# Optimization experiments

Hardware: AMD Instinct MI355X
Metric: run time of the kernel (lower is better)

Reference implementation:

```python
import jax, jax.numpy as jnp
import numpy as np

H = 12        # num_heads
BLOCK = 128   # sliding-window block_size (include_adjacent=True)
EPS = 1e-5


def layer_norm(x, s, b):
    m = x.mean(-1, keepdims=True)
    v = ((x - m) ** 2).mean(-1, keepdims=True)
    return (x - m) * jax.lax.rsqrt(v + EPS) * s + b


def setup_inputs() -> dict:
    key = jax.random.key(0)
    V, D, F, L, B, S, C = 32000, 768, 3072, 4, 8, 1024, 2
    ks = jax.random.split(key, 10)
    r = lambda k, shp: jax.random.normal(k, shp, dtype=jnp.float32) * 0.02
    return {
        "tokens": jax.random.randint(ks[0], (B, S), 0, V),
        "mask": jnp.ones((B, S), dtype=jnp.int32),
        "emb": r(ks[1], (V, D)),
        "in_w": r(ks[2], (L, 3 * D, D)),
        "in_b": jnp.zeros((L, 3 * D), jnp.float32),
        "out_w": r(ks[3], (L, D, D)),
        "out_b": jnp.zeros((L, D), jnp.float32),
        "ln1_s": jnp.ones((L, D), jnp.float32),
        "ln1_b": jnp.zeros((L, D), jnp.float32),
        "ln2_s": jnp.ones((L, D), jnp.float32),
        "ln2_b": jnp.zeros((L, D), jnp.float32),
        "ff_w1": r(ks[4], (L, F, D)),
        "ff_b1": jnp.zeros((L, F), jnp.float32),
        "ff_w2": r(ks[5], (L, D, F)),
        "ff_b2": jnp.zeros((L, D), jnp.float32),
        "pool_w": r(ks[6], (1, D)),
        "pool_b": jnp.zeros((1,), jnp.float32),
        "cls_ln_s": jnp.ones((D,), jnp.float32),
        "cls_ln_b": jnp.zeros((D,), jnp.float32),
        "cls_w1": r(ks[7], (D, D)),
        "cls_b1": jnp.zeros((D,), jnp.float32),
        "cls_w2": r(ks[8], (C, D)),
        "cls_b2": jnp.zeros((C,), jnp.float32),
    }


def reference(tokens, mask, emb, in_w, in_b, out_w, out_b, ln1_s, ln1_b, ln2_s, ln2_b,
              ff_w1, ff_b1, ff_w2, ff_b2, pool_w, pool_b, cls_ln_s, cls_ln_b,
              cls_w1, cls_b1, cls_w2, cls_b2):
    B, S = tokens.shape
    D = emb.shape[1]
    L = in_w.shape[0]
    hd = D // H
    neg = jnp.finfo(jnp.float32).min

    x = emb[tokens]  # [B,S,D]
    # sinusoidal positional encoding (eval mode: dropout = identity)
    pos = jnp.arange(S, dtype=jnp.float32)[:, None]
    div = jnp.exp(jnp.arange(0, D, 2, dtype=jnp.float32) * (-np.log(10000.0) / D))
    pe = (jnp.zeros((S, D), jnp.float32)
          .at[:, 0::2].set(jnp.sin(pos * div))
          .at[:, 1::2].set(jnp.cos(pos * div)))
    x = x + pe[None]

    idx = jnp.arange(S)
    band = jnp.abs(idx[None, :] - idx[:, None]) <= BLOCK        # [S,S] allowed band
    kpm = (mask != 0)                                            # [B,S] valid keys
    allowed = band[None] & kpm[:, None, :]                       # [B,S,S]

    all_w = []
    for l in range(L):
        h = layer_norm(x, ln1_s[l], ln1_b[l])
        qkv = h @ in_w[l].T + in_b[l]                            # [B,S,3D]
        q, k, v = jnp.split(qkv, 3, axis=-1)
        q = q.reshape(B, S, H, hd).transpose(0, 2, 1, 3) * (1.0 / np.sqrt(hd))
        k = k.reshape(B, S, H, hd).transpose(0, 2, 1, 3)
        v = v.reshape(B, S, H, hd).transpose(0, 2, 1, 3)
        scores = jnp.einsum('bhqd,bhkd->bhqk', q, k)             # [B,H,S,S]
        scores = jnp.where(allowed[:, None], scores, neg)
        w = jax.nn.softmax(scores, axis=-1)
        attn = jnp.einsum('bhqk,bhkd->bhqd', w, v)
        attn = attn.transpose(0, 2, 1, 3).reshape(B, S, D)
        attn = attn @ out_w[l].T + out_b[l]
        x = x + attn
        h2 = layer_norm(x, ln2_s[l], ln2_b[l])
        ff = jax.nn.gelu(h2 @ ff_w1[l].T + ff_b1[l], approximate=False)
        ff = ff @ ff_w2[l].T + ff_b2[l]
        x = x + ff
        all_w.append(w.mean(axis=1))                             # head-averaged [B,S,S]

    # attention pooling
    sc = (x @ pool_w.T + pool_b)[..., 0]                         # [B,S]
    sc = jnp.where(mask == 0, neg, sc)
    pw = jax.nn.softmax(sc, axis=-1)[..., None]
    pooled = jnp.sum(pw * x, axis=1)                             # [B,D]
    pooled = jnp.tanh(pooled)
    c = layer_norm(pooled, cls_ln_s, cls_ln_b)
    c = jnp.tanh(c @ cls_w1.T + cls_b1)
    out = c @ cls_w2.T + cls_b2                                  # [B,2]
    return out, jnp.stack(all_w)
```

## Files before the change

### kernel.cpp

```cpp
#include <hip/hip_runtime.h>
#include <math.h>

#define S_LEN 1024
#define D_MODEL 768
#define NHEAD 12
#define NEG_INF -3.4028234663852886e38f

#define QT 32
#define KB 288

typedef _Float16 f16x8 __attribute__((ext_vector_type(8)));
typedef __attribute__((ext_vector_type(4))) float f32x4;

typedef const __attribute__((address_space(1))) unsigned int ga_u32;
typedef __attribute__((address_space(3))) unsigned int ls_u32;
__device__ __forceinline__ void gload16(const void* g, void* l) {
  __builtin_amdgcn_global_load_lds((ga_u32*)g, (ls_u32*)l, 16, 0, 0);
}

__device__ __forceinline__ float gelu_exact(float v) {
  return 0.5f * v * (1.0f + erff(v * 0.7071067811865475f));
}
__device__ __forceinline__ unsigned short f2h(float f) {
  union { _Float16 h; unsigned short u; } x; x.h = (_Float16)f; return x.u;
}

__global__ __launch_bounds__(256) void embed_kernel(
    const int* __restrict__ tok, const float* __restrict__ emb,
    float* __restrict__ X, int total) {
  int i = blockIdx.x * 256 + threadIdx.x;
  if (i >= total) return;
  int d = i % D_MODEL;
  int bs = i / D_MODEL;
  int s = bs & (S_LEN - 1);
  int t = tok[bs];
  float div = expf((float)(d & ~1) * (-9.210340371976184f / 768.0f));
  float ang = (float)s * div;
  float pe = (d & 1) ? cosf(ang) : sinf(ang);
  X[i] = emb[(size_t)t * D_MODEL + d] + pe;
}

__global__ __launch_bounds__(256) void cvt_w_h(
    const float* __restrict__ W, unsigned short* __restrict__ H, int n4) {
  int i = blockIdx.x * 256 + threadIdx.x;
  if (i >= n4) return;
  float4 w = ((const float4*)W)[i];
  ushort4 h;
  h.x = f2h(w.x); h.y = f2h(w.y); h.z = f2h(w.z); h.w = f2h(w.w);
  ((ushort4*)H)[i] = h;
}

__global__ __launch_bounds__(256) void ln_kernel(
    const float* __restrict__ X, const float* __restrict__ gam,
    const float* __restrict__ bet, unsigned short* __restrict__ Y) {
  __shared__ float scratch[4];
  const int row = blockIdx.x;
  const int tid = threadIdx.x;
  const float* xr = X + (size_t)row * D_MODEL;
  float v0 = xr[tid], v1 = xr[tid + 256], v2 = xr[tid + 512];
  float s = v0 + v1 + v2;
#pragma unroll
  for (int o = 32; o; o >>= 1) s += __shfl_xor(s, o, 64);
  if ((tid & 63) == 0) scratch[tid >> 6] = s;
  __syncthreads();
  float mean = (scratch[0] + scratch[1] + scratch[2] + scratch[3]) * (1.0f / 768.0f);
  __syncthreads();
  float d0 = v0 - mean, d1 = v1 - mean, d2 = v2 - mean;
  float ss = d0 * d0 + d1 * d1 + d2 * d2;
#pragma unroll
  for (int o = 32; o; o >>= 1) ss += __shfl_xor(ss, o, 64);
  if ((tid & 63) == 0) scratch[tid >> 6] = ss;
  __syncthreads();
  float var = (scratch[0] + scratch[1] + scratch[2] + scratch[3]) * (1.0f / 768.0f);
  float rstd = rsqrtf(var + 1e-5f);
  unsigned short* yr = Y + (size_t)row * D_MODEL;
  yr[tid]       = f2h(d0 * rstd * gam[tid]       + bet[tid]);
  yr[tid + 256] = f2h(d1 * rstd * gam[tid + 256] + bet[tid + 256]);
  yr[tid + 512] = f2h(d2 * rstd * gam[tid + 512] + bet[tid + 512]);
}

template <int EPI>
__global__ __launch_bounds__(256) void gemm128(
    const unsigned short* __restrict__ A, const unsigned short* __restrict__ W,
    const float* __restrict__ bias, void* __restrict__ Cv,
    int N, int K, int NX) {
  __shared__ __align__(16) unsigned short SH[24576];
  const int tid = threadIdx.x;
  const int nwg = gridDim.x;
  const int wg = ((blockIdx.x & 7) * (nwg >> 3)) + (blockIdx.x >> 3);
  const int SX = NX >> 1;
  const int st = wg >> 4, w16 = wg & 15;
  const int ty = (st / SX) * 8 + (w16 >> 1);
  const int tx = (st % SX) * 2 + (w16 & 1);
  const int m0 = ty << 7, n0 = tx << 7;
  const int wave = tid >> 6, lane = tid & 63;
  const int wr = (wave >> 1) << 6, wc = (wave & 1) << 6;
  const int lq = lane >> 4, lr = lane & 15;
  const int rA0 = (wave << 5) + (lane >> 2);
  const int rA1 = rA0 + 16;
  const int sl = lane & 3;
  const size_t gA0 = (size_t)(m0 + rA0) * K + ((sl ^ ((rA0 >> 1) & 3)) << 3);
  const size_t gA1 = (size_t)(m0 + rA1) * K + ((sl ^ ((rA1 >> 1) & 3)) << 3);
  const size_t gB0 = (size_t)(n0 + rA0) * K + ((sl ^ ((rA0 >> 1) & 3)) << 3);
  const size_t gB1 = (size_t)(n0 + rA1) * K + ((sl ^ ((rA1 >> 1) & 3)) << 3);
  const int lws = wave << 10;

  const int nt = K >> 5;
  auto stage = [&](int buf, int t) {
    unsigned short* base = SH + (buf << 13);
    const int kk = t << 5;
    gload16(A + gA0 + kk, base + lws);
    gload16(A + gA1 + kk, base + lws + 512);
    gload16(W + gB0 + kk, base + 4096 + lws);
    gload16(W + gB1 + kk, base + 4096 + lws + 512);
  };
  stage(0, 0);
  stage(1, 1);

  f32x4 acc[4][4] = {};
  int cb = 0;
  for (int t = 0; t < nt; ++t) {
    if (t + 1 < nt) {
      asm volatile("s_waitcnt vmcnt(4)" ::: "memory");
    } else {
      asm volatile("s_waitcnt vmcnt(0)" ::: "memory");
    }
    __builtin_amdgcn_s_barrier();
    __builtin_amdgcn_sched_barrier(0);
    const unsigned short* As = SH + (cb << 13);
    const unsigned short* Bs = As + 4096;
    f16x8 af[4], bq[4];
#pragma unroll
    for (int i = 0; i < 4; ++i) {
      int r = wr + (i << 4) + lr;
      af[i] = *(const f16x8*)&As[r * 32 + ((lq ^ ((r >> 1) & 3)) << 3)];
    }
#pragma unroll
    for (int j = 0; j < 4; ++j) {
      int r = wc + (j << 4) + lr;
      bq[j] = *(const f16x8*)&Bs[r * 32 + ((lq ^ ((r >> 1) & 3)) << 3)];
    }
    if (t + 2 < nt) {
      int sb = cb + 2; if (sb >= 3) sb -= 3;
      stage(sb, t + 2);
    }
    __builtin_amdgcn_sched_barrier(0);
    __builtin_amdgcn_s_setprio(1);
#pragma unroll
    for (int i = 0; i < 4; ++i)
#pragma unroll
      for (int j = 0; j < 4; ++j)
        acc[i][j] = __builtin_amdgcn_mfma_f32_16x16x32_f16(af[i], bq[j], acc[i][j], 0, 0, 0);
    __builtin_amdgcn_s_setprio(0);
    cb = (cb == 2) ? 0 : cb + 1;
  }
  float bval[4];
#pragma unroll
  for (int j = 0; j < 4; ++j) bval[j] = bias[n0 + wc + (j << 4) + lr];

  if (EPI == 2) {
    float* C = (float*)Cv;
#pragma unroll
    for (int j = 0; j < 4; ++j) {
      const int gcol = n0 + wc + (j << 4) + lr;
#pragma unroll
      for (int i = 0; i < 4; ++i) {
        const int grow0 = m0 + wr + (i << 4) + (lq << 2);
#pragma unroll
        for (int r = 0; r < 4; ++r) {
          size_t off = (size_t)(grow0 + r) * N + gcol;
          C[off] += acc[i][j][r] + bval[j];
        }
      }
    }
    return;
  }

  unsigned short* C = (unsigned short*)Cv;
  __syncthreads();
#pragma unroll
  for (int hh = 0; hh < 2; ++hh) {
    if ((wave >> 1) == hh) {
#pragma unroll
      for (int i = 0; i < 4; ++i)
#pragma unroll
        for (int j = 0; j < 4; ++j) {
          const int colb = wc + (j << 4) + lr;
#pragma unroll
          for (int r = 0; r < 4; ++r) {
            const int rowl = (i << 4) + (lq << 2) + r;
            float v = acc[i][j][r] + bval[j];
            if (EPI == 1) v = gelu_exact(v);
            const int ch = (colb >> 3) ^ (rowl & 7);
            SH[rowl * 128 + (ch << 3) + (colb & 7)] = f2h(v);
          }
        }
    }
    __syncthreads();
#pragma unroll
    for (int it = 0; it < 4; ++it) {
      const int cid = tid + (it << 8);
      const int row = cid >> 4, ch = cid & 15;
      uint4 v8 = *(uint4*)&SH[row * 128 + ((ch ^ (row & 7)) << 3)];
      *(uint4*)&C[(size_t)(m0 + (hh << 6) + row) * N + n0 + (ch << 3)] = v8;
    }
    __syncthreads();
  }
}

__global__ __launch_bounds__(512) void attn_kernel(
    const unsigned short* __restrict__ qkv, const int* __restrict__ mask,
    unsigned short* __restrict__ attn_out, float* __restrict__ allw) {
  __shared__ __align__(16) unsigned short Ks[KB * 72];
  __shared__ __align__(16) unsigned short Vt[64 * 328];
  __shared__ __align__(16) unsigned short Qs[32 * 72];
  __shared__ __align__(16) unsigned short Ps[32 * 328];
  __shared__ __align__(16) float redmax[2][16][4];
  __shared__ __align__(16) float redsum[2][16][4];
  __shared__ int kvalid[KB];

  const int qt0 = blockIdx.y * QT;
  const int b = blockIdx.x;
  const int tid = threadIdx.x;
  const int w = tid >> 6, lane = tid & 63;
  const int lr = lane & 15, lg = lane >> 4;
  const int k0 = qt0 - 128;
  const int qh = w & 1, wq = w >> 1;
  const int nkt = (wq < 2) ? 5 : 4;

  for (int j = tid; j < KB; j += 512) {
    int key = k0 + j;
    kvalid[j] = (key >= 0 && key < S_LEN && mask[b * S_LEN + key] != 0) ? 1 : 0;
  }

  f32x4 pm[5] = {};
  const size_t rowbase = (size_t)(b * S_LEN) * 2304;
  const int qloc = lg << 2;
  const int qbase = (qh << 4) + qloc;

  for (int h = 0; h < NHEAD; ++h) {
    const int hoff = h << 6;
    if (tid < 256) {
      int r = tid >> 3, c = tid & 7;
      uint4 v = *(const uint4*)(qkv + rowbase + (size_t)(qt0 + r) * 2304 + hoff + (c << 3));
      *(uint4*)&Qs[r * 72 + ((c ^ (r & 7)) << 3)] = v;
    }
    for (int idx = tid; idx < 2304; idx += 512) {
      int r = idx >> 3, c = idx & 7;
      int key = k0 + r;
      uint4 kv = {0, 0, 0, 0}, vv = {0, 0, 0, 0};
      if ((unsigned)key < (unsigned)S_LEN) {
        const unsigned short* base = qkv + rowbase + (size_t)key * 2304 + hoff + (c << 3);
        kv = *(const uint4*)(base + 768);
        vv = *(const uint4*)(base + 1536);
      }
      *(uint4*)&Ks[r * 72 + ((c ^ (r & 7)) << 3)] = kv;
      const unsigned short* ve = (const unsigned short*)&vv;
      int jc = r >> 3, jw = r & 7;
#pragma unroll
      for (int e = 0; e < 8; ++e) {
        int d = (c << 3) + e;
        Vt[d * 328 + ((jc ^ ((d >> 2) & 7)) << 3) + jw] = ve[e];
      }
    }
    __syncthreads();

    f16x8 aq[2];
#pragma unroll
    for (int kc = 0; kc < 2; ++kc) {
      int r = (qh << 4) + lr;
      aq[kc] = *(f16x8*)&Qs[r * 72 + ((((kc << 2) + lg) ^ (r & 7)) << 3)];
    }
    f32x4 sc[5];
    __builtin_amdgcn_s_setprio(1);
#pragma unroll
    for (int t = 0; t < 5; ++t) {
      sc[t] = (f32x4){0.0f, 0.0f, 0.0f, 0.0f};
      if (t < nkt) {
        int r = ((wq + (t << 2)) << 4) + lr;
#pragma unroll
        for (int kc = 0; kc < 2; ++kc) {
          f16x8 bk = *(f16x8*)&Ks[r * 72 + ((((kc << 2) + lg) ^ (r & 7)) << 3)];
          sc[t] = __builtin_amdgcn_mfma_f32_16x16x32_f16(aq[kc], bk, sc[t], 0, 0, 0);
        }
      }
    }
    __builtin_amdgcn_s_setprio(0);
#pragma unroll
    for (int t = 0; t < 5; ++t) if (t < nkt) {
      int j = ((wq + (t << 2)) << 4) + lr;
      int okk = kvalid[j];
#pragma unroll
      for (int rg = 0; rg < 4; ++rg) {
        int q = qbase + rg;
        float s = sc[t][rg] * 0.125f;
        sc[t][rg] = (okk && j >= q && j <= q + 256) ? s : NEG_INF;
      }
    }
    float mx[4], zs[4];
#pragma unroll
    for (int rg = 0; rg < 4; ++rg) {
      float m = NEG_INF;
#pragma unroll
      for (int t = 0; t < 5; ++t) if (t < nkt) m = fmaxf(m, sc[t][rg]);
      mx[rg] = m;
    }
#pragma unroll
    for (int o = 1; o < 16; o <<= 1)
#pragma unroll
      for (int rg = 0; rg < 4; ++rg) mx[rg] = fmaxf(mx[rg], __shfl_xor(mx[rg], o, 64));
    if (lr == 0)
#pragma unroll
      for (int rg = 0; rg < 4; ++rg) redmax[qh][qloc + rg][wq] = mx[rg];
    __syncthreads();
#pragma unroll
    for (int rg = 0; rg < 4; ++rg) {
      f32x4 v = *(f32x4*)&redmax[qh][qloc + rg][0];
      mx[rg] = fmaxf(fmaxf(v[0], v[1]), fmaxf(v[2], v[3]));
      zs[rg] = 0.0f;
    }
#pragma unroll
    for (int t = 0; t < 5; ++t) if (t < nkt)
#pragma unroll
      for (int rg = 0; rg < 4; ++rg) {
        float e = expf(sc[t][rg] - mx[rg]);
        sc[t][rg] = e;
        zs[rg] += e;
      }
#pragma unroll
    for (int o = 1; o < 16; o <<= 1)
#pragma unroll
      for (int rg = 0; rg < 4; ++rg) zs[rg] += __shfl_xor(zs[rg], o, 64);
    if (lr == 0)
#pragma unroll
      for (int rg = 0; rg < 4; ++rg) redsum[qh][qloc + rg][wq] = zs[rg];
    __syncthreads();
#pragma unroll
    for (int rg = 0; rg < 4; ++rg) {
      f32x4 v = *(f32x4*)&redsum[qh][qloc + rg][0];
      zs[rg] = 1.0f / (v[0] + v[1] + v[2] + v[3]);
    }
#pragma unroll
    for (int t = 0; t < 5; ++t) if (t < nkt) {
      int j = ((wq + (t << 2)) << 4) + lr;
      int pc = j >> 3, pw = j & 7;
#pragma unroll
      for (int rg = 0; rg < 4; ++rg) {
        float p = sc[t][rg] * zs[rg];
        pm[t][rg] += p;
        int row = qbase + rg;
        Ps[row * 328 + ((pc ^ (row & 7)) << 3) + pw] = f2h(p);
      }
    }
    __syncthreads();
    {
      const int qt = w >> 2, dt = w & 3;
      const int ra = (qt << 4) + lr;
      const int rd = (dt << 4) + lr;
      f32x4 o4 = {0.0f, 0.0f, 0.0f, 0.0f};
      __builtin_amdgcn_s_setprio(1);
#pragma unroll
      for (int ks = 0; ks < 9; ++ks) {
        f16x8 pa = *(f16x8*)&Ps[ra * 328 + ((((ks << 2) + lg) ^ (ra & 7)) << 3)];
        f16x8 vb = *(f16x8*)&Vt[rd * 328 + ((((ks << 2) + lg) ^ ((rd >> 2) & 7)) << 3)];
        o4 = __builtin_amdgcn_mfma_f32_16x16x32_f16(pa, vb, o4, 0, 0, 0);
      }
      __builtin_amdgcn_s_setprio(0);
      unsigned short* op = attn_out +
          ((size_t)(b * S_LEN + qt0 + (qt << 4) + (lg << 2))) * D_MODEL + hoff + (dt << 4) + lr;
#pragma unroll
      for (int rg = 0; rg < 4; ++rg) op[(size_t)rg * D_MODEL] = f2h(o4[rg]);
    }
    __syncthreads();
  }

#pragma unroll
  for (int t = 0; t < 5; ++t) if (t < nkt) {
    int j = ((wq + (t << 2)) << 4) + lr;
    int key = k0 + j;
    if ((unsigned)key < (unsigned)S_LEN) {
      float* ap = allw + ((size_t)(b * S_LEN) + qt0 + qbase) * S_LEN + key;
#pragma unroll
      for (int rg = 0; rg < 4; ++rg) ap[(size_t)rg * S_LEN] = pm[t][rg] * (1.0f / 12.0f);
    }
  }
}

__global__ __launch_bounds__(256) void pool_score(
    const float* __restrict__ X, const int* __restrict__ mask,
    const float* __restrict__ pool_w, const float* __restrict__ pool_b,
    float* __restrict__ sc) {
  const int tid = threadIdx.x;
  const int wave = tid >> 6, lane = tid & 63;
  const int row = blockIdx.x * 4 + wave;
  const float* xr = X + (size_t)row * D_MODEL;
  float acc = 0.0f;
#pragma unroll
  for (int c = 0; c < 3; ++c) {
    int d = (lane << 2) + (c << 8);
    float4 xv = *(const float4*)(xr + d);
    float4 wv = *(const float4*)(pool_w + d);
    acc += xv.x * wv.x + xv.y * wv.y + xv.z * wv.z + xv.w * wv.w;
  }
#pragma unroll
  for (int o = 32; o; o >>= 1) acc += __shfl_xor(acc, o, 64);
  if (lane == 0)
    sc[row] = (mask[row] == 0) ? NEG_INF : (acc + pool_b[0]);
}

__global__ __launch_bounds__(256) void pool_softmax(float* __restrict__ sc) {
  __shared__ float scratch[4];
  __shared__ float buf[S_LEN];
  const int b = blockIdx.x;
  const int tid = threadIdx.x;
  float* sb = sc + b * S_LEN;
  float m = NEG_INF;
  for (int s = tid; s < S_LEN; s += 256) { buf[s] = sb[s]; m = fmaxf(m, buf[s]); }
#pragma unroll
  for (int o = 32; o; o >>= 1) m = fmaxf(m, __shfl_xor(m, o, 64));
  if ((tid & 63) == 0) scratch[tid >> 6] = m;
  __syncthreads();
  m = fmaxf(fmaxf(scratch[0], scratch[1]), fmaxf(scratch[2], scratch[3]));
  __syncthreads();
  float z = 0.0f;
  for (int s = tid; s < S_LEN; s += 256) { float e = expf(buf[s] - m); buf[s] = e; z += e; }
#pragma unroll
  for (int o = 32; o; o >>= 1) z += __shfl_xor(z, o, 64);
  if ((tid & 63) == 0) scratch[tid >> 6] = z;
  __syncthreads();
  float Z = scratch[0] + scratch[1] + scratch[2] + scratch[3];
  const float inv = 1.0f / Z;
  for (int s = tid; s < S_LEN; s += 256) sb[s] = buf[s] * inv;
}

__global__ __launch_bounds__(256) void pool_sum(
    const float* __restrict__ X, const float* __restrict__ wgt,
    float* __restrict__ partial) {
  const int bx = blockIdx.x;
  const int b = blockIdx.y;
  const int dchunk = bx >> 3, schunk = bx & 7;
  const int d = (dchunk << 8) + threadIdx.x;
  const int s0 = schunk << 7;
  const float* xb = X + ((size_t)(b << 10) + s0) * D_MODEL + d;
  const float* wb = wgt + (b << 10) + s0;
  float acc = 0.0f;
  for (int s = 0; s < 128; ++s) acc += wb[s] * xb[(size_t)s * D_MODEL];
  partial[((size_t)((b << 3) + schunk)) * D_MODEL + d] = acc;
}

__global__ __launch_bounds__(256) void cls_ln(
    const float* __restrict__ partial,
    const float* __restrict__ ln_s, const float* __restrict__ ln_b,
    float* __restrict__ cbuf_g) {
  const int b = blockIdx.x;
  const int tid = threadIdx.x;
  __shared__ float scratch[4];
  __shared__ __align__(16) float pbuf[D_MODEL];
  for (int d = tid; d < D_MODEL; d += 256) {
    float acc = 0.0f;
#pragma unroll
    for (int p = 0; p < 8; ++p) acc += partial[((size_t)((b << 3) + p)) * D_MODEL + d];
    pbuf[d] = tanhf(acc);
  }
  __syncthreads();
  float ls = 0.0f;
  for (int d = tid; d < D_MODEL; d += 256) ls += pbuf[d];
#pragma unroll
  for (int o = 32; o; o >>= 1) ls += __shfl_xor(ls, o, 64);
  if ((tid & 63) == 0) scratch[tid >> 6] = ls;
  __syncthreads();
  float mean = (scratch[0] + scratch[1] + scratch[2] + scratch[3]) * (1.0f / 768.0f);
  __syncthreads();
  float vs = 0.0f;
  for (int d = tid; d < D_MODEL; d += 256) { float dd = pbuf[d] - mean; vs += dd * dd; }
#pragma unroll
  for (int o = 32; o; o >>= 1) vs += __shfl_xor(vs, o, 64);
  if ((tid & 63) == 0) scratch[tid >> 6] = vs;
  __syncthreads();
  float var = (scratch[0] + scratch[1] + scratch[2] + scratch[3]) * (1.0f / 768.0f);
  float rstd = rsqrtf(var + 1e-5f);
  for (int d = tid; d < D_MODEL; d += 256)
    cbuf_g[b * D_MODEL + d] = (pbuf[d] - mean) * rstd * ln_s[d] + ln_b[d];
}

__global__ __launch_bounds__(256) void cls_mlp1(
    const float* __restrict__ cbuf_g, const float* __restrict__ w1,
    const float* __restrict__ b1, float* __restrict__ c1_g) {
  const int tid = threadIdx.x;
  const int wave = tid >> 6, lane = tid & 63;
  const int i = blockIdx.x * 4 + wave;
  const int b = blockIdx.y;
  __shared__ __align__(16) float cb[D_MODEL];
  for (int d = tid; d < D_MODEL; d += 256) cb[d] = cbuf_g[b * D_MODEL + d];
  __syncthreads();
  const float* wr = w1 + (size_t)i * D_MODEL;
  float acc = 0.0f;
#pragma unroll
  for (int c = 0; c < 3; ++c) {
    int d = (lane << 2) + (c << 8);
    float4 wv = *(const float4*)(wr + d);
    float4 cv = *(const float4*)(&cb[d]);
    acc += wv.x * cv.x + wv.y * cv.y + wv.z * cv.z + wv.w * cv.w;
  }
#pragma unroll
  for (int o = 32; o; o >>= 1) acc += __shfl_xor(acc, o, 64);
  if (lane == 0) c1_g[b * D_MODEL + i] = tanhf(acc + b1[i]);
}

__global__ __launch_bounds__(256) void cls_logits(
    const float* __restrict__ c1_g, const float* __restrict__ w2,
    const float* __restrict__ b2, float* __restrict__ out) {
  const int b = blockIdx.x;
  const int tid = threadIdx.x;
  __shared__ float scratch[4];
#pragma unroll
  for (int jc = 0; jc < 2; ++jc) {
    float acc = 0.0f;
    for (int i = tid; i < D_MODEL; i += 256) acc += c1_g[b * D_MODEL + i] * w2[jc * D_MODEL + i];
#pragma unroll
    for (int o = 32; o; o >>= 1) acc += __shfl_xor(acc, o, 64);
    if ((tid & 63) == 0) scratch[tid >> 6] = acc;
    __syncthreads();
    if (tid == 0) out[b * 2 + jc] = scratch[0] + scratch[1] + scratch[2] + scratch[3] + b2[jc];
    __syncthreads();
  }
}

extern "C" void kernel_launch(void* const* d_in, const int* in_sizes, int n_in,
                              void* d_out, int out_size, void* d_ws, size_t ws_size,
                              hipStream_t stream) {
  const int*   tokens  = (const int*)d_in[0];
  const int*   mask    = (const int*)d_in[1];
  const float* emb     = (const float*)d_in[2];
  const float* in_w    = (const float*)d_in[3];
  const float* in_b    = (const float*)d_in[4];
  const float* out_w   = (const float*)d_in[5];
  const float* out_b   = (const float*)d_in[6];
  const float* ln1_s   = (const float*)d_in[7];
  const float* ln1_b   = (const float*)d_in[8];
  const float* ln2_s   = (const float*)d_in[9];
  const float* ln2_b   = (const float*)d_in[10];
  const float* ff_w1   = (const float*)d_in[11];
  const float* ff_b1   = (const float*)d_in[12];
  const float* ff_w2   = (const float*)d_in[13];
  const float* ff_b2   = (const float*)d_in[14];
  const float* pool_w  = (const float*)d_in[15];
  const float* pool_b  = (const float*)d_in[16];
  const float* cls_ln_s = (const float*)d_in[17];
  const float* cls_ln_b = (const float*)d_in[18];
  const float* cls_w1  = (const float*)d_in[19];
  const float* cls_b1  = (const float*)d_in[20];
  const float* cls_w2  = (const float*)d_in[21];
  const float* cls_b2  = (const float*)d_in[22];

  float* outp = (float*)d_out;
  float* ws = (float*)d_ws;
  const size_t XN = (size_t)8 * 1024 * 768;
  const size_t BIGU = (size_t)8192 * 3072;
  float* x = ws;
  unsigned short* bigu = (unsigned short*)(ws + XN);
  unsigned short* h_f16 = (unsigned short*)(ws + XN + BIGU / 2);
  unsigned short* wall = h_f16 + XN;
  unsigned short* wall_in  = wall;
  unsigned short* wall_out = wall + (size_t)7077888;
  unsigned short* wall_ff1 = wall + (size_t)9437184;
  unsigned short* wall_ff2 = wall + (size_t)18874368;
  float* clsbuf = (float*)(wall + (size_t)28311552);
  float* sc_ws = clsbuf;
  float* partial = clsbuf + 8192;
  float* cbuf_ws = partial + 49152;
  float* c1_ws = cbuf_ws + 6144;
  float* allw = outp + 16;

  hipMemsetAsync(d_out, 0, (size_t)out_size * sizeof(float), stream);

  cvt_w_h<<<6912, 256, 0, stream>>>(in_w,  wall_in,  1769472);
  cvt_w_h<<<2304, 256, 0, stream>>>(out_w, wall_out,  589824);
  cvt_w_h<<<9216, 256, 0, stream>>>(ff_w1, wall_ff1, 2359296);
  cvt_w_h<<<9216, 256, 0, stream>>>(ff_w2, wall_ff2, 2359296);

  const int total = (int)XN;
  embed_kernel<<<(total + 255) / 256, 256, 0, stream>>>(tokens, emb, x, total);

  for (int l = 0; l < 4; ++l) {
    ln_kernel<<<8192, 256, 0, stream>>>(x, ln1_s + l * 768, ln1_b + l * 768, h_f16);
    gemm128<0><<<1152, 256, 0, stream>>>(h_f16, wall_in + (size_t)l * 1769472,
                                         in_b + l * 2304, bigu, 2304, 768, 18);
    attn_kernel<<<dim3(8, S_LEN / QT), 512, 0, stream>>>(bigu, mask, h_f16,
                                                         allw + (size_t)l * 8 * 1024 * 1024);
    gemm128<2><<<384, 256, 0, stream>>>(h_f16, wall_out + (size_t)l * 589824,
                                        out_b + l * 768, x, 768, 768, 6);
    ln_kernel<<<8192, 256, 0, stream>>>(x, ln2_s + l * 768, ln2_b + l * 768, h_f16);
    gemm128<1><<<1536, 256, 0, stream>>>(h_f16, wall_ff1 + (size_t)l * 2359296,
                                         ff_b1 + l * 3072, bigu, 3072, 768, 24);
    gemm128<2><<<384, 256, 0, stream>>>(bigu, wall_ff2 + (size_t)l * 2359296,
                                        ff_b2 + l * 768, x, 768, 3072, 6);
  }

  pool_score<<<2048, 256, 0, stream>>>(x, mask, pool_w, pool_b, sc_ws);
  pool_softmax<<<8, 256, 0, stream>>>(sc_ws);
  pool_sum<<<dim3(24, 8), 256, 0, stream>>>(x, sc_ws, partial);
  cls_ln<<<8, 256, 0, stream>>>(partial, cls_ln_s, cls_ln_b, cbuf_ws);
  cls_mlp1<<<dim3(192, 8), 256, 0, stream>>>(cbuf_ws, cls_w1, cls_b1, c1_ws);
  cls_logits<<<8, 256, 0, stream>>>(c1_ws, cls_w2, cls_b2, outp);
}
```

Before: 1.351 ms.

## Write V transposed from QKV GEMM epilogue and load pre-transposed V in attention

The QKV projection GEMM gains an epilogue variant that writes the V third of its output, transposed, into a separate [B, D, S] buffer through shared memory. The attention kernel then loads V rows with vectorized 16-byte copies instead of scattering eight 2-byte stores per element into its transposed shared tile. This removes the per-element LDS transpose in attention, which runs for every head. The cost is a transposed store path in the GEMM for the V columns and extra workspace placed after the QKV region.

```diff
diff --git a/kernel.cpp b/kernel.cpp
--- a/kernel.cpp
+++ b/kernel.cpp
@@ -83,7 +83,7 @@
 __global__ __launch_bounds__(256) void gemm128(
     const unsigned short* __restrict__ A, const unsigned short* __restrict__ W,
     const float* __restrict__ bias, void* __restrict__ Cv,
-    int N, int K, int NX) {
+    unsigned short* __restrict__ VtG, int N, int K, int NX) {
   __shared__ __align__(16) unsigned short SH[24576];
   const int tid = threadIdx.x;
   const int nwg = gridDim.x;
@@ -176,6 +176,33 @@
     return;
   }
 
+  if (EPI == 3 && n0 >= 1536) {
+    __syncthreads();
+#pragma unroll
+    for (int i = 0; i < 4; ++i)
+#pragma unroll
+      for (int j = 0; j < 4; ++j) {
+        const int colb = wc + (j << 4) + lr;
+#pragma unroll
+        for (int r = 0; r < 4; ++r) {
+          const int rowg = wr + (i << 4) + (lq << 2) + r;
+          float v = acc[i][j][r] + bval[j];
+          SH[colb * 128 + (((rowg >> 3) ^ (colb & 7)) << 3) + (rowg & 7)] = f2h(v);
+        }
+      }
+    __syncthreads();
+    const int bidx = m0 >> 10, s0 = m0 & 1023;
+    unsigned short* vg = VtG + ((size_t)bidx * 768 + (n0 - 1536)) * 1024 + s0;
+#pragma unroll
+    for (int it = 0; it < 8; ++it) {
+      const int cid = tid + (it << 8);
+      const int col = cid >> 4, ch = cid & 15;
+      uint4 v8 = *(uint4*)&SH[col * 128 + ((ch ^ (col & 7)) << 3)];
+      *(uint4*)&vg[(size_t)col * 1024 + (ch << 3)] = v8;
+    }
+    return;
+  }
+
   unsigned short* C = (unsigned short*)Cv;
   __syncthreads();
 #pragma unroll
@@ -209,7 +236,8 @@
 }
 
 __global__ __launch_bounds__(512) void attn_kernel(
-    const unsigned short* __restrict__ qkv, const int* __restrict__ mask,
+    const unsigned short* __restrict__ qkv, const unsigned short* __restrict__ VtG,
+    const int* __restrict__ mask,
     unsigned short* __restrict__ attn_out, float* __restrict__ allw) {
   __shared__ __align__(16) unsigned short Ks[KB * 72];
   __shared__ __align__(16) unsigned short Vt[64 * 328];
@@ -237,6 +265,7 @@
   const size_t rowbase = (size_t)(b * S_LEN) * 2304;
   const int qloc = lg << 2;
   const int qbase = (qh << 4) + qloc;
+  const int vd = tid >> 3, vs8 = tid & 7;
 
   for (int h = 0; h < NHEAD; ++h) {
     const int hoff = h << 6;
@@ -248,19 +277,18 @@
     for (int idx = tid; idx < 2304; idx += 512) {
       int r = idx >> 3, c = idx & 7;
       int key = k0 + r;
-      uint4 kv = {0, 0, 0, 0}, vv = {0, 0, 0, 0};
-      if ((unsigned)key < (unsigned)S_LEN) {
-        const unsigned short* base = qkv + rowbase + (size_t)key * 2304 + hoff + (c << 3);
-        kv = *(const uint4*)(base + 768);
-        vv = *(const uint4*)(base + 1536);
-      }
+      uint4 kv = {0, 0, 0, 0};
+      if ((unsigned)key < (unsigned)S_LEN)
+        kv = *(const uint4*)(qkv + rowbase + (size_t)key * 2304 + hoff + 768 + (c << 3));
       *(uint4*)&Ks[r * 72 + ((c ^ (r & 7)) << 3)] = kv;
-      const unsigned short* ve = (const unsigned short*)&vv;
-      int jc = r >> 3, jw = r & 7;
-#pragma unroll
-      for (int e = 0; e < 8; ++e) {
-        int d = (c << 3) + e;
-        Vt[d * 328 + ((jc ^ ((d >> 2) & 7)) << 3) + jw] = ve[e];
+    }
+    {
+      const unsigned short* vg = VtG + ((size_t)b * 768 + hoff) * 1024 + (size_t)vd * 1024;
+      for (int c = vs8; c < 36; c += 8) {
+        int key = k0 + (c << 3);
+        uint4 v = {0, 0, 0, 0};
+        if ((unsigned)key < (unsigned)S_LEN) v = *(const uint4*)(vg + key);
+        *(uint4*)&Vt[vd * 328 + ((c ^ ((vd >> 2) & 7)) << 3)] = v;
       }
     }
     __syncthreads();
@@ -559,6 +587,7 @@
   const size_t BIGU = (size_t)8192 * 3072;
   float* x = ws;
   unsigned short* bigu = (unsigned short*)(ws + XN);
+  unsigned short* vtg = bigu + (size_t)8192 * 2304;
   unsigned short* h_f16 = (unsigned short*)(ws + XN + BIGU / 2);
   unsigned short* wall = h_f16 + XN;
   unsigned short* wall_in  = wall;
@@ -584,17 +613,17 @@
 
   for (int l = 0; l < 4; ++l) {
     ln_kernel<<<8192, 256, 0, stream>>>(x, ln1_s + l * 768, ln1_b + l * 768, h_f16);
-    gemm128<0><<<1152, 256, 0, stream>>>(h_f16, wall_in + (size_t)l * 1769472,
-                                         in_b + l * 2304, bigu, 2304, 768, 18);
-    attn_kernel<<<dim3(8, S_LEN / QT), 512, 0, stream>>>(bigu, mask, h_f16,
+    gemm128<3><<<1152, 256, 0, stream>>>(h_f16, wall_in + (size_t)l * 1769472,
+                                         in_b + l * 2304, bigu, vtg, 2304, 768, 18);
+    attn_kernel<<<dim3(8, S_LEN / QT), 512, 0, stream>>>(bigu, vtg, mask, h_f16,
                                                          allw + (size_t)l * 8 * 1024 * 1024);
     gemm128<2><<<384, 256, 0, stream>>>(h_f16, wall_out + (size_t)l * 589824,
-                                        out_b + l * 768, x, 768, 768, 6);
+                                        out_b + l * 768, x, nullptr, 768, 768, 6);
     ln_kernel<<<8192, 256, 0, stream>>>(x, ln2_s + l * 768, ln2_b + l * 768, h_f16);
     gemm128<1><<<1536, 256, 0, stream>>>(h_f16, wall_ff1 + (size_t)l * 2359296,
-                                         ff_b1 + l * 3072, bigu, 3072, 768, 24);
+                                         ff_b1 + l * 3072, bigu, nullptr, 3072, 768, 24);
     gemm128<2><<<384, 256, 0, stream>>>(bigu, wall_ff2 + (size_t)l * 2359296,
-                                        ff_b2 + l * 768, x, 768, 3072, 6);
+                                        ff_b2 + l * 768, x, nullptr, 768, 3072, 6);
   }
 
   pool_score<<<2048, 256, 0, stream>>>(x, mask, pool_w, pool_b, sc_ws);
```

New measurement: 1.368 ms. No clear change (+1.2%).
